# Kernel tuning notes

Hardware: AMD Instinct MI355X
Metric: run time of the kernel (lower is better)

The kernel has to match this reference:

```python
import jax, jax.numpy as jnp
import numpy as np

N_NODES = 50000
N_EDGES = 800000
D = 64


def setup_inputs() -> dict:
    key = jax.random.key(0)
    ks = jax.random.split(key, 8)
    x = jax.random.normal(ks[0], (N_NODES, D), dtype=jnp.float32)
    edge_index = jax.random.randint(ks[1], (2, N_EDGES), 0, N_NODES, dtype=jnp.int64)
    # GCNConv params (PyG: Linear without bias inside lin, bias added after aggregation)
    def glorot(k, fan_in, fan_out):
        lim = (6.0 / (fan_in + fan_out)) ** 0.5
        return jax.random.uniform(k, (fan_in, fan_out), jnp.float32, -lim, lim)
    W1 = glorot(ks[2], D, D); b1 = jnp.zeros((D,), jnp.float32)
    W2 = glorot(ks[3], D, D); b2 = jnp.zeros((D,), jnp.float32)
    W3 = glorot(ks[4], D, D); b3 = jnp.zeros((D,), jnp.float32)
    return {"x": x, "edge_index": edge_index,
            "W1": W1, "b1": b1, "W2": W2, "b2": b2, "W3": W3, "b3": b3}


def _gcn_norm(edge_index, n_nodes, dtype):
    # Add self-loops, compute symmetric normalization D^-1/2 (A+I) D^-1/2 (PyG GCNConv default).
    loop = jnp.arange(n_nodes, dtype=edge_index.dtype)
    src = jnp.concatenate([edge_index[0], loop])  # message source j
    dst = jnp.concatenate([edge_index[1], loop])  # aggregation target i
    deg = jax.ops.segment_sum(jnp.ones_like(dst, dtype=dtype), dst, num_segments=n_nodes)
    dinv = jnp.where(deg > 0, jax.lax.rsqrt(deg), 0.0)
    norm = dinv[src] * dinv[dst]  # [E + N]
    return src, dst, norm


def _gcn_conv(x, src, dst, norm, W, b, n_nodes):
    h = x @ W                              # [N, D_out]
    msg = h[src] * norm[:, None]           # gather + scale, [E+N, D_out]
    out = jax.ops.segment_sum(msg, dst, num_segments=n_nodes)  # scatter-add
    return out + b


def reference(x, edge_index, W1, b1, W2, b2, W3, b3):
    n = x.shape[0]
    src, dst, norm = _gcn_norm(edge_index, n, x.dtype)
    # layer 0: conv -> relu -> residual
    h = _gcn_conv(x, src, dst, norm, W1, b1, n)
    h = jax.nn.relu(h) + x
    # layer 1: conv -> relu -> residual
    r = h
    h = _gcn_conv(h, src, dst, norm, W2, b2, n)
    h = jax.nn.relu(h) + r
    # layer 2 (final): conv only
    h = _gcn_conv(h, src, dst, norm, W3, b3, n)
    return h
```

## Files before the change

kernel.cpp:

```cpp
#include <hip/hip_runtime.h>
#include <hip/hip_bf16.h>


#define CAP 64
#define EDGE_CHUNK 1024

typedef __attribute__((ext_vector_type(8))) short bf16x8;
typedef __attribute__((ext_vector_type(4))) float f32x4;

__device__ inline unsigned pack_bf16(float a, float b) {
    union { float f; unsigned i; } ua, ub;
    ua.f = a; ub.f = b;
    unsigned x = (ua.i + 0x7fffu + ((ua.i >> 16) & 1u)) >> 16;
    unsigned y = (ub.i + 0x7fffu + ((ub.i >> 16) & 1u)) >> 16;
    return x | (y << 16);
}
__device__ inline unsigned short to_bf16(float a) {
    union { float f; unsigned i; } u; u.f = a;
    return (unsigned short)((u.i + 0x7fffu + ((u.i >> 16) & 1u)) >> 16);
}
__device__ inline void acc_bf16x2(unsigned u, float& a, float& b) {
    union { unsigned i; float f; } lo, hi;
    lo.i = u << 16;
    hi.i = u & 0xffff0000u;
    a += lo.f; b += hi.f;
}

__global__ void fill_kernel(const int* __restrict__ src, const int* __restrict__ dst,
                            int* __restrict__ cnt, int* __restrict__ adj,
                            int E, int npc) {
    int cls = blockIdx.x & 7;
    int base = (blockIdx.x >> 3) * EDGE_CHUNK;
    int end = min(base + EDGE_CHUNK, E);
    int lo = cls * npc, hi = lo + npc;
    for (int e = base + threadIdx.x; e < end; e += blockDim.x) {
        int d = dst[e];
        if (d >= lo && d < hi) {
            int p = atomicAdd(&cnt[d], 1);
            adj[(size_t)d * CAP + p] = src[e];
        }
    }
}

__device__ inline void stage_W(const float* __restrict__ W, unsigned short* Wb, int t) {
#pragma unroll
    for (int e0 = 0; e0 < 2; e0++) {
        int e = t + e0 * 256;
        int sc = e >> 6;
        int l  = e & 63;
        int s = sc >> 2, c = sc & 3;
        int nn = c * 16 + (l & 15);
        int kb = s * 32 + (l >> 4) * 8;
        const float* wp = &W[(size_t)kb * 64 + nn];
        unsigned q0 = pack_bf16(wp[0 * 64], wp[1 * 64]);
        unsigned q1 = pack_bf16(wp[2 * 64], wp[3 * 64]);
        unsigned q2 = pack_bf16(wp[4 * 64], wp[5 * 64]);
        unsigned q3 = pack_bf16(wp[6 * 64], wp[7 * 64]);
        *(uint4*)&Wb[e * 8] = make_uint4(q0, q1, q2, q3);
    }
}

__global__ __launch_bounds__(256) void gemm_kernel(const float* __restrict__ in,
                                                   const float* __restrict__ W,
                                                   const int* __restrict__ cnt,
                                                   unsigned short* __restrict__ g, int n) {
    __shared__ unsigned short Wb[512 * 8];
    int t = threadIdx.x;
    stage_W(W, Wb, t);

    int wv = t >> 6;
    int lane = t & 63;
    int quad = lane >> 4;
    int m16 = lane & 15;

    int rowA = blockIdx.x * 64 + wv * 16 + m16;
    union { bf16x8 v; uint4 u; } a0, a1;
    {
        float4 f0 = make_float4(0, 0, 0, 0), f1 = f0, f2 = f0, f3 = f0;
        if (rowA < n) {
            const float* rp = &in[(size_t)rowA * 64];
            f0 = *(const float4*)&rp[quad * 8];
            f1 = *(const float4*)&rp[quad * 8 + 4];
            f2 = *(const float4*)&rp[32 + quad * 8];
            f3 = *(const float4*)&rp[32 + quad * 8 + 4];
        }
        a0.u = make_uint4(pack_bf16(f0.x, f0.y), pack_bf16(f0.z, f0.w),
                          pack_bf16(f1.x, f1.y), pack_bf16(f1.z, f1.w));
        a1.u = make_uint4(pack_bf16(f2.x, f2.y), pack_bf16(f2.z, f2.w),
                          pack_bf16(f3.x, f3.y), pack_bf16(f3.z, f3.w));
    }
    __syncthreads();

    f32x4 acc[4];
#pragma unroll
    for (int c = 0; c < 4; c++) {
        bf16x8 b0 = *(const bf16x8*)&Wb[((size_t)(0 * 4 + c) * 64 + lane) * 8];
        bf16x8 b1 = *(const bf16x8*)&Wb[((size_t)(1 * 4 + c) * 64 + lane) * 8];
        f32x4 z = {0.f, 0.f, 0.f, 0.f};
        z = __builtin_amdgcn_mfma_f32_16x16x32_bf16(a0.v, b0, z, 0, 0, 0);
        z = __builtin_amdgcn_mfma_f32_16x16x32_bf16(a1.v, b1, z, 0, 0, 0);
        acc[c] = z;
    }

    int rowbase = blockIdx.x * 64 + wv * 16 + quad * 4;
    float dv[4];
#pragma unroll
    for (int r = 0; r < 4; r++) {
        int row = rowbase + r;
        dv[r] = (row < n) ? rsqrtf((float)(cnt[row] + 1)) : 0.f;
    }
#pragma unroll
    for (int c = 0; c < 4; c++) {
#pragma unroll
        for (int r = 0; r < 4; r++) {
            int row = rowbase + r;
            if (row < n)
                g[(size_t)row * 64 + c * 16 + m16] = to_bf16(acc[c][r] * dv[r]);
        }
    }
}

template <int WRITE_H>
__global__ __launch_bounds__(256, 4) void aggemm_kernel(
        const unsigned short* __restrict__ g_in,
        const int* __restrict__ cnt,
        const int* __restrict__ adj,
        const float* __restrict__ bias,
        const float* __restrict__ res,
        const float* __restrict__ W,
        float* __restrict__ h_out,
        unsigned short* __restrict__ g_out,
        int n) {
    __shared__ unsigned short Wb[512 * 8];
    __shared__ unsigned short Afrag[256 * 8];
    __shared__ float dsh[32];
    int t = threadIdx.x;

    int r  = t >> 3;
    int lg = t & 7;
    const int c8 = lg * 8;
    int i = blockIdx.x * 32 + r;
    float v0 = 0.f, v1 = 0.f, v2 = 0.f, v3 = 0.f;
    float v4 = 0.f, v5 = 0.f, v6 = 0.f, v7 = 0.f;
    float dvv = 0.f;
    if (i < n) {
        int deg = cnt[i];
        const int* lst = adj + (size_t)i * CAP;
        float4 rr0 = *(const float4*)&res[(size_t)i * 64 + c8];
        float4 rr1 = *(const float4*)&res[(size_t)i * 64 + c8 + 4];
        float a0 = 0.f, a1 = 0.f, a2 = 0.f, a3 = 0.f;
        float a4 = 0.f, a5 = 0.f, a6 = 0.f, a7 = 0.f;
        {
            uint4 v = *(const uint4*)&g_in[(size_t)i * 64 + c8];
            acc_bf16x2(v.x, a0, a1); acc_bf16x2(v.y, a2, a3);
            acc_bf16x2(v.z, a4, a5); acc_bf16x2(v.w, a6, a7);
        }
        int nfull = deg >> 3;
        int4 ja, jb;
        if (nfull > 0) { ja = *(const int4*)&lst[0]; jb = *(const int4*)&lst[4]; }
        for (int b = 0; b < nfull; b++) {
            int4 na = ja, nb = jb;
            if (b + 1 < nfull) {
                na = *(const int4*)&lst[(b + 1) * 8];
                nb = *(const int4*)&lst[(b + 1) * 8 + 4];
            }
            uint4 w0 = *(const uint4*)&g_in[(size_t)ja.x * 64 + c8];
            uint4 w1 = *(const uint4*)&g_in[(size_t)ja.y * 64 + c8];
            uint4 w2 = *(const uint4*)&g_in[(size_t)ja.z * 64 + c8];
            uint4 w3 = *(const uint4*)&g_in[(size_t)ja.w * 64 + c8];
            uint4 w4 = *(const uint4*)&g_in[(size_t)jb.x * 64 + c8];
            uint4 w5 = *(const uint4*)&g_in[(size_t)jb.y * 64 + c8];
            uint4 w6 = *(const uint4*)&g_in[(size_t)jb.z * 64 + c8];
            uint4 w7 = *(const uint4*)&g_in[(size_t)jb.w * 64 + c8];
            acc_bf16x2(w0.x, a0, a1); acc_bf16x2(w0.y, a2, a3);
            acc_bf16x2(w0.z, a4, a5); acc_bf16x2(w0.w, a6, a7);
            acc_bf16x2(w1.x, a0, a1); acc_bf16x2(w1.y, a2, a3);
            acc_bf16x2(w1.z, a4, a5); acc_bf16x2(w1.w, a6, a7);
            acc_bf16x2(w2.x, a0, a1); acc_bf16x2(w2.y, a2, a3);
            acc_bf16x2(w2.z, a4, a5); acc_bf16x2(w2.w, a6, a7);
            acc_bf16x2(w3.x, a0, a1); acc_bf16x2(w3.y, a2, a3);
            acc_bf16x2(w3.z, a4, a5); acc_bf16x2(w3.w, a6, a7);
            acc_bf16x2(w4.x, a0, a1); acc_bf16x2(w4.y, a2, a3);
            acc_bf16x2(w4.z, a4, a5); acc_bf16x2(w4.w, a6, a7);
            acc_bf16x2(w5.x, a0, a1); acc_bf16x2(w5.y, a2, a3);
            acc_bf16x2(w5.z, a4, a5); acc_bf16x2(w5.w, a6, a7);
            acc_bf16x2(w6.x, a0, a1); acc_bf16x2(w6.y, a2, a3);
            acc_bf16x2(w6.z, a4, a5); acc_bf16x2(w6.w, a6, a7);
            acc_bf16x2(w7.x, a0, a1); acc_bf16x2(w7.y, a2, a3);
            acc_bf16x2(w7.z, a4, a5); acc_bf16x2(w7.w, a6, a7);
            ja = na; jb = nb;
        }
        int k = nfull * 8;
        if (k + 4 <= deg) {
            int4 j4 = *(const int4*)&lst[k];
            uint4 w0 = *(const uint4*)&g_in[(size_t)j4.x * 64 + c8];
            uint4 w1 = *(const uint4*)&g_in[(size_t)j4.y * 64 + c8];
            uint4 w2 = *(const uint4*)&g_in[(size_t)j4.z * 64 + c8];
            uint4 w3 = *(const uint4*)&g_in[(size_t)j4.w * 64 + c8];
            acc_bf16x2(w0.x, a0, a1); acc_bf16x2(w0.y, a2, a3);
            acc_bf16x2(w0.z, a4, a5); acc_bf16x2(w0.w, a6, a7);
            acc_bf16x2(w1.x, a0, a1); acc_bf16x2(w1.y, a2, a3);
            acc_bf16x2(w1.z, a4, a5); acc_bf16x2(w1.w, a6, a7);
            acc_bf16x2(w2.x, a0, a1); acc_bf16x2(w2.y, a2, a3);
            acc_bf16x2(w2.z, a4, a5); acc_bf16x2(w2.w, a6, a7);
            acc_bf16x2(w3.x, a0, a1); acc_bf16x2(w3.y, a2, a3);
            acc_bf16x2(w3.z, a4, a5); acc_bf16x2(w3.w, a6, a7);
            k += 4;
        }
        for (; k < deg; k++) {
            uint4 v = *(const uint4*)&g_in[(size_t)lst[k] * 64 + c8];
            acc_bf16x2(v.x, a0, a1); acc_bf16x2(v.y, a2, a3);
            acc_bf16x2(v.z, a4, a5); acc_bf16x2(v.w, a6, a7);
        }
        dvv = rsqrtf((float)(deg + 1));
        float4 b0 = *(const float4*)&bias[c8];
        float4 b1 = *(const float4*)&bias[c8 + 4];
        v0 = fmaxf(dvv * a0 + b0.x, 0.f) + rr0.x;
        v1 = fmaxf(dvv * a1 + b0.y, 0.f) + rr0.y;
        v2 = fmaxf(dvv * a2 + b0.z, 0.f) + rr0.z;
        v3 = fmaxf(dvv * a3 + b0.w, 0.f) + rr0.w;
        v4 = fmaxf(dvv * a4 + b1.x, 0.f) + rr1.x;
        v5 = fmaxf(dvv * a5 + b1.y, 0.f) + rr1.y;
        v6 = fmaxf(dvv * a6 + b1.z, 0.f) + rr1.z;
        v7 = fmaxf(dvv * a7 + b1.w, 0.f) + rr1.w;
        if (WRITE_H) {
            *(float4*)&h_out[(size_t)i * 64 + c8]     = make_float4(v0, v1, v2, v3);
            *(float4*)&h_out[(size_t)i * 64 + c8 + 4] = make_float4(v4, v5, v6, v7);
        }
    }
    stage_W(W, Wb, t);
    {
        uint4 pk;
        pk.x = pack_bf16(v0, v1);
        pk.y = pack_bf16(v2, v3);
        pk.z = pack_bf16(v4, v5);
        pk.w = pack_bf16(v6, v7);
        int sA = r >> 4, mA = r & 15;
        *(uint4*)&Afrag[((size_t)(sA * 8 + lg) * 16 + mA) * 8] = pk;
        if (lg == 0) dsh[r] = dvv;
    }
    __syncthreads();

    int wv = t >> 6;
    int lane = t & 63;
    int quad = lane >> 4;
    int m16 = lane & 15;
    int sB = wv & 1;
    int ch = wv >> 1;
    bf16x8 af0 = *(const bf16x8*)&Afrag[((size_t)(sB * 8 + quad) * 16 + m16) * 8];
    bf16x8 af1 = *(const bf16x8*)&Afrag[((size_t)(sB * 8 + 4 + quad) * 16 + m16) * 8];
    f32x4 acc[2];
#pragma unroll
    for (int c2 = 0; c2 < 2; c2++) {
        int c = ch * 2 + c2;
        bf16x8 b0 = *(const bf16x8*)&Wb[((size_t)(0 * 4 + c) * 64 + lane) * 8];
        bf16x8 b1 = *(const bf16x8*)&Wb[((size_t)(1 * 4 + c) * 64 + lane) * 8];
        f32x4 z = {0.f, 0.f, 0.f, 0.f};
        z = __builtin_amdgcn_mfma_f32_16x16x32_bf16(af0, b0, z, 0, 0, 0);
        z = __builtin_amdgcn_mfma_f32_16x16x32_bf16(af1, b1, z, 0, 0, 0);
        acc[c2] = z;
    }
    int lrow = sB * 16 + quad * 4;
    int rowbase = blockIdx.x * 32 + lrow;
    float dv2[4];
#pragma unroll
    for (int rr = 0; rr < 4; rr++)
        dv2[rr] = dsh[lrow + rr];
#pragma unroll
    for (int c2 = 0; c2 < 2; c2++) {
        int c = ch * 2 + c2;
#pragma unroll
        for (int rr = 0; rr < 4; rr++) {
            int row = rowbase + rr;
            if (row < n)
                g_out[(size_t)row * 64 + c * 16 + m16] = to_bf16(acc[c2][rr] * dv2[rr]);
        }
    }
}

__global__ __launch_bounds__(256, 4) void agg_kernel(const unsigned short* __restrict__ g,
                                                     const int* __restrict__ cnt,
                                                     const int* __restrict__ adj,
                                                     const float* __restrict__ bias,
                                                     float* __restrict__ out, int n) {
    int t = threadIdx.x;
    int lg = t & 7;
    int i = blockIdx.x * 32 + (t >> 3);
    if (i >= n) return;
    int deg = cnt[i];
    const int* lst = adj + (size_t)i * CAP;
    const int c8 = lg * 8;
    size_t rowoff = (size_t)i * 64 + c8;
    float a0 = 0.f, a1 = 0.f, a2 = 0.f, a3 = 0.f;
    float a4 = 0.f, a5 = 0.f, a6 = 0.f, a7 = 0.f;
    {
        uint4 v = *(const uint4*)&g[(size_t)i * 64 + c8];
        acc_bf16x2(v.x, a0, a1); acc_bf16x2(v.y, a2, a3);
        acc_bf16x2(v.z, a4, a5); acc_bf16x2(v.w, a6, a7);
    }
    int nfull = deg >> 3;
    int4 ja, jb;
    if (nfull > 0) { ja = *(const int4*)&lst[0]; jb = *(const int4*)&lst[4]; }
    for (int b = 0; b < nfull; b++) {
        int4 na = ja, nb = jb;
        if (b + 1 < nfull) {
            na = *(const int4*)&lst[(b + 1) * 8];
            nb = *(const int4*)&lst[(b + 1) * 8 + 4];
        }
        uint4 v0 = *(const uint4*)&g[(size_t)ja.x * 64 + c8];
        uint4 v1 = *(const uint4*)&g[(size_t)ja.y * 64 + c8];
        uint4 v2 = *(const uint4*)&g[(size_t)ja.z * 64 + c8];
        uint4 v3 = *(const uint4*)&g[(size_t)ja.w * 64 + c8];
        uint4 v4 = *(const uint4*)&g[(size_t)jb.x * 64 + c8];
        uint4 v5 = *(const uint4*)&g[(size_t)jb.y * 64 + c8];
        uint4 v6 = *(const uint4*)&g[(size_t)jb.z * 64 + c8];
        uint4 v7 = *(const uint4*)&g[(size_t)jb.w * 64 + c8];
        acc_bf16x2(v0.x, a0, a1); acc_bf16x2(v0.y, a2, a3);
        acc_bf16x2(v0.z, a4, a5); acc_bf16x2(v0.w, a6, a7);
        acc_bf16x2(v1.x, a0, a1); acc_bf16x2(v1.y, a2, a3);
        acc_bf16x2(v1.z, a4, a5); acc_bf16x2(v1.w, a6, a7);
        acc_bf16x2(v2.x, a0, a1); acc_bf16x2(v2.y, a2, a3);
        acc_bf16x2(v2.z, a4, a5); acc_bf16x2(v2.w, a6, a7);
        acc_bf16x2(v3.x, a0, a1); acc_bf16x2(v3.y, a2, a3);
        acc_bf16x2(v3.z, a4, a5); acc_bf16x2(v3.w, a6, a7);
        acc_bf16x2(v4.x, a0, a1); acc_bf16x2(v4.y, a2, a3);
        acc_bf16x2(v4.z, a4, a5); acc_bf16x2(v4.w, a6, a7);
        acc_bf16x2(v5.x, a0, a1); acc_bf16x2(v5.y, a2, a3);
        acc_bf16x2(v5.z, a4, a5); acc_bf16x2(v5.w, a6, a7);
        acc_bf16x2(v6.x, a0, a1); acc_bf16x2(v6.y, a2, a3);
        acc_bf16x2(v6.z, a4, a5); acc_bf16x2(v6.w, a6, a7);
        acc_bf16x2(v7.x, a0, a1); acc_bf16x2(v7.y, a2, a3);
        acc_bf16x2(v7.z, a4, a5); acc_bf16x2(v7.w, a6, a7);
        ja = na; jb = nb;
    }
    int k = nfull * 8;
    if (k + 4 <= deg) {
        int4 j4 = *(const int4*)&lst[k];
        uint4 v0 = *(const uint4*)&g[(size_t)j4.x * 64 + c8];
        uint4 v1 = *(const uint4*)&g[(size_t)j4.y * 64 + c8];
        uint4 v2 = *(const uint4*)&g[(size_t)j4.z * 64 + c8];
        uint4 v3 = *(const uint4*)&g[(size_t)j4.w * 64 + c8];
        acc_bf16x2(v0.x, a0, a1); acc_bf16x2(v0.y, a2, a3);
        acc_bf16x2(v0.z, a4, a5); acc_bf16x2(v0.w, a6, a7);
        acc_bf16x2(v1.x, a0, a1); acc_bf16x2(v1.y, a2, a3);
        acc_bf16x2(v1.z, a4, a5); acc_bf16x2(v1.w, a6, a7);
        acc_bf16x2(v2.x, a0, a1); acc_bf16x2(v2.y, a2, a3);
        acc_bf16x2(v2.z, a4, a5); acc_bf16x2(v2.w, a6, a7);
        acc_bf16x2(v3.x, a0, a1); acc_bf16x2(v3.y, a2, a3);
        acc_bf16x2(v3.z, a4, a5); acc_bf16x2(v3.w, a6, a7);
        k += 4;
    }
    for (; k < deg; k++) {
        uint4 v = *(const uint4*)&g[(size_t)lst[k] * 64 + c8];
        acc_bf16x2(v.x, a0, a1); acc_bf16x2(v.y, a2, a3);
        acc_bf16x2(v.z, a4, a5); acc_bf16x2(v.w, a6, a7);
    }
    float dv = rsqrtf((float)(deg + 1));
    float4 b0 = *(const float4*)&bias[c8];
    float4 b1 = *(const float4*)&bias[c8 + 4];
    float4 o0, o1;
    o0.x = dv * a0 + b0.x; o0.y = dv * a1 + b0.y;
    o0.z = dv * a2 + b0.z; o0.w = dv * a3 + b0.w;
    o1.x = dv * a4 + b1.x; o1.y = dv * a5 + b1.y;
    o1.z = dv * a6 + b1.z; o1.w = dv * a7 + b1.w;
    *(float4*)&out[rowoff] = o0;
    *(float4*)&out[rowoff + 4] = o1;
}

extern "C" void kernel_launch(void* const* d_in, const int* in_sizes, int n_in,
                              void* d_out, int out_size, void* d_ws, size_t ws_size,
                              hipStream_t stream) {
    const float* x  = (const float*)d_in[0];
    const int*   ei = (const int*)d_in[1];
    const float* W1 = (const float*)d_in[2];
    const float* b1 = (const float*)d_in[3];
    const float* W2 = (const float*)d_in[4];
    const float* b2 = (const float*)d_in[5];
    const float* W3 = (const float*)d_in[6];
    const float* b3 = (const float*)d_in[7];
    float* out = (float*)d_out;

    const int N = in_sizes[0] / 64;
    const int E = in_sizes[1] / 2;
    const int* src = ei;
    const int* dst = ei + E;
    const int npc = (N + 7) / 8;
    const int nEdgeChunks = (E + EDGE_CHUNK - 1) / EDGE_CHUNK;

    char* p = (char*)d_ws;
    int*            cnt = (int*)p;            p += ((N + 63) / 64) * 64 * 4;
    int*            adj = (int*)p;            p += ((size_t)N + 1) * CAP * 4;
    unsigned short* ga  = (unsigned short*)p; p += (size_t)N * 64 * 2;
    unsigned short* gb  = (unsigned short*)p; p += (size_t)N * 64 * 2;
    float*          h1  = (float*)p;          p += (size_t)N * 64 * 4;

    const int tileBlocks = (N + 63) / 64;
    const int halfBlocks = (N + 31) / 32;

    hipMemsetAsync(cnt, 0, (size_t)N * 4, stream);
    fill_kernel<<<nEdgeChunks * 8, 256, 0, stream>>>(src, dst, cnt, adj, E, npc);

    gemm_kernel<<<tileBlocks, 256, 0, stream>>>(x, W1, cnt, ga, N);
    aggemm_kernel<1><<<halfBlocks, 256, 0, stream>>>(ga, cnt, adj, b1, x, W2, h1, gb, N);
    aggemm_kernel<0><<<halfBlocks, 256, 0, stream>>>(gb, cnt, adj, b2, h1, W3, nullptr, ga, N);
    agg_kernel<<<halfBlocks, 256, 0, stream>>>(ga, cnt, adj, b3, out, N);
}
```

Measured before the change: 182.4 us.

## Software-pipeline neighbor gathers, stage GEMM outputs through LDS, store residual as bf16

The per-row neighbor gather moves into a shared helper that prefetches the next batch of eight neighbor rows and the index batch after that while the current batch accumulates, to hide gather latency. The GEMM and fused agg-GEMM kernels now stage their bf16 output tile in shared memory and write full 16-byte rows, replacing the earlier scattered 2-byte stores. The intermediate residual h1 is kept as bf16 instead of fp32, halving its write and read traffic at some cost in precision. The gemm kernel also gets a launch-bounds occupancy hint, and extra barriers are added to reuse shared buffers.

```diff
diff --git a/kernel.cpp b/kernel.cpp
--- a/kernel.cpp
+++ b/kernel.cpp
@@ -24,6 +24,83 @@
     lo.i = u << 16;
     hi.i = u & 0xffff0000u;
     a += lo.f; b += hi.f;
+}
+
+__device__ inline void gather_rows(const unsigned short* __restrict__ g,
+                                   const int* __restrict__ lst, int deg, int c8,
+                                   float& a0, float& a1, float& a2, float& a3,
+                                   float& a4, float& a5, float& a6, float& a7) {
+    int nfull = deg >> 3;
+    int4 ja, jb, na, nb;
+    uint4 w0, w1, w2, w3, w4, w5, w6, w7;
+    if (nfull > 0) {
+        ja = *(const int4*)&lst[0]; jb = *(const int4*)&lst[4];
+        w0 = *(const uint4*)&g[(size_t)ja.x * 64 + c8];
+        w1 = *(const uint4*)&g[(size_t)ja.y * 64 + c8];
+        w2 = *(const uint4*)&g[(size_t)ja.z * 64 + c8];
+        w3 = *(const uint4*)&g[(size_t)ja.w * 64 + c8];
+        w4 = *(const uint4*)&g[(size_t)jb.x * 64 + c8];
+        w5 = *(const uint4*)&g[(size_t)jb.y * 64 + c8];
+        w6 = *(const uint4*)&g[(size_t)jb.z * 64 + c8];
+        w7 = *(const uint4*)&g[(size_t)jb.w * 64 + c8];
+        if (nfull > 1) { na = *(const int4*)&lst[8]; nb = *(const int4*)&lst[12]; }
+    }
+    for (int b = 0; b < nfull; b++) {
+        bool has1 = (b + 1 < nfull);
+        bool has2 = (b + 2 < nfull);
+        int4 ta, tb;
+        if (has2) {
+            ta = *(const int4*)&lst[(b + 2) * 8];
+            tb = *(const int4*)&lst[(b + 2) * 8 + 4];
+        }
+        acc_bf16x2(w0.x, a0, a1); acc_bf16x2(w0.y, a2, a3);
+        acc_bf16x2(w0.z, a4, a5); acc_bf16x2(w0.w, a6, a7);
+        if (has1) w0 = *(const uint4*)&g[(size_t)na.x * 64 + c8];
+        acc_bf16x2(w1.x, a0, a1); acc_bf16x2(w1.y, a2, a3);
+        acc_bf16x2(w1.z, a4, a5); acc_bf16x2(w1.w, a6, a7);
+        if (has1) w1 = *(const uint4*)&g[(size_t)na.y * 64 + c8];
+        acc_bf16x2(w2.x, a0, a1); acc_bf16x2(w2.y, a2, a3);
+        acc_bf16x2(w2.z, a4, a5); acc_bf16x2(w2.w, a6, a7);
+        if (has1) w2 = *(const uint4*)&g[(size_t)na.z * 64 + c8];
+        acc_bf16x2(w3.x, a0, a1); acc_bf16x2(w3.y, a2, a3);
+        acc_bf16x2(w3.z, a4, a5); acc_bf16x2(w3.w, a6, a7);
+        if (has1) w3 = *(const uint4*)&g[(size_t)na.w * 64 + c8];
+        acc_bf16x2(w4.x, a0, a1); acc_bf16x2(w4.y, a2, a3);
+        acc_bf16x2(w4.z, a4, a5); acc_bf16x2(w4.w, a6, a7);
+        if (has1) w4 = *(const uint4*)&g[(size_t)nb.x * 64 + c8];
+        acc_bf16x2(w5.x, a0, a1); acc_bf16x2(w5.y, a2, a3);
+        acc_bf16x2(w5.z, a4, a5); acc_bf16x2(w5.w, a6, a7);
+        if (has1) w5 = *(const uint4*)&g[(size_t)nb.y * 64 + c8];
+        acc_bf16x2(w6.x, a0, a1); acc_bf16x2(w6.y, a2, a3);
+        acc_bf16x2(w6.z, a4, a5); acc_bf16x2(w6.w, a6, a7);
+        if (has1) w6 = *(const uint4*)&g[(size_t)nb.z * 64 + c8];
+        acc_bf16x2(w7.x, a0, a1); acc_bf16x2(w7.y, a2, a3);
+        acc_bf16x2(w7.z, a4, a5); acc_bf16x2(w7.w, a6, a7);
+        if (has1) w7 = *(const uint4*)&g[(size_t)nb.w * 64 + c8];
+        if (has2) { na = ta; nb = tb; }
+    }
+    int k = nfull * 8;
+    if (k + 4 <= deg) {
+        int4 j4 = *(const int4*)&lst[k];
+        uint4 t0 = *(const uint4*)&g[(size_t)j4.x * 64 + c8];
+        uint4 t1 = *(const uint4*)&g[(size_t)j4.y * 64 + c8];
+        uint4 t2 = *(const uint4*)&g[(size_t)j4.z * 64 + c8];
+        uint4 t3 = *(const uint4*)&g[(size_t)j4.w * 64 + c8];
+        acc_bf16x2(t0.x, a0, a1); acc_bf16x2(t0.y, a2, a3);
+        acc_bf16x2(t0.z, a4, a5); acc_bf16x2(t0.w, a6, a7);
+        acc_bf16x2(t1.x, a0, a1); acc_bf16x2(t1.y, a2, a3);
+        acc_bf16x2(t1.z, a4, a5); acc_bf16x2(t1.w, a6, a7);
+        acc_bf16x2(t2.x, a0, a1); acc_bf16x2(t2.y, a2, a3);
+        acc_bf16x2(t2.z, a4, a5); acc_bf16x2(t2.w, a6, a7);
+        acc_bf16x2(t3.x, a0, a1); acc_bf16x2(t3.y, a2, a3);
+        acc_bf16x2(t3.z, a4, a5); acc_bf16x2(t3.w, a6, a7);
+        k += 4;
+    }
+    for (; k < deg; k++) {
+        uint4 v = *(const uint4*)&g[(size_t)lst[k] * 64 + c8];
+        acc_bf16x2(v.x, a0, a1); acc_bf16x2(v.y, a2, a3);
+        acc_bf16x2(v.z, a4, a5); acc_bf16x2(v.w, a6, a7);
+    }
 }
 
 __global__ void fill_kernel(const int* __restrict__ src, const int* __restrict__ dst,
@@ -60,10 +137,10 @@
     }
 }
 
-__global__ __launch_bounds__(256) void gemm_kernel(const float* __restrict__ in,
-                                                   const float* __restrict__ W,
-                                                   const int* __restrict__ cnt,
-                                                   unsigned short* __restrict__ g, int n) {
+__global__ __launch_bounds__(256, 4) void gemm_kernel(const float* __restrict__ in,
+                                                      const float* __restrict__ W,
+                                                      const int* __restrict__ cnt,
+                                                      unsigned short* __restrict__ g, int n) {
     __shared__ unsigned short Wb[512 * 8];
     int t = threadIdx.x;
     stage_W(W, Wb, t);
@@ -102,37 +179,46 @@
         acc[c] = z;
     }
 
-    int rowbase = blockIdx.x * 64 + wv * 16 + quad * 4;
+    int lrow = wv * 16 + quad * 4;
     float dv[4];
 #pragma unroll
     for (int r = 0; r < 4; r++) {
-        int row = rowbase + r;
+        int row = blockIdx.x * 64 + lrow + r;
         dv[r] = (row < n) ? rsqrtf((float)(cnt[row] + 1)) : 0.f;
     }
+    __syncthreads();
+    unsigned short* Ofrag = Wb;
 #pragma unroll
     for (int c = 0; c < 4; c++) {
 #pragma unroll
-        for (int r = 0; r < 4; r++) {
-            int row = rowbase + r;
-            if (row < n)
-                g[(size_t)row * 64 + c * 16 + m16] = to_bf16(acc[c][r] * dv[r]);
-        }
-    }
-}
-
-template <int WRITE_H>
+        for (int r = 0; r < 4; r++)
+            Ofrag[(size_t)(lrow + r) * 64 + c * 16 + m16] = to_bf16(acc[c][r] * dv[r]);
+    }
+    __syncthreads();
+#pragma unroll
+    for (int it = 0; it < 2; it++) {
+        int unit = t + it * 256;
+        int row = unit >> 3, chv = unit & 7;
+        int grow = blockIdx.x * 64 + row;
+        if (grow < n)
+            *(uint4*)&g[(size_t)grow * 64 + chv * 8] =
+                *(const uint4*)&Ofrag[(size_t)row * 64 + chv * 8];
+    }
+}
+
+template <int WRITE_H, int RES_BF16>
 __global__ __launch_bounds__(256, 4) void aggemm_kernel(
         const unsigned short* __restrict__ g_in,
         const int* __restrict__ cnt,
         const int* __restrict__ adj,
         const float* __restrict__ bias,
-        const float* __restrict__ res,
+        const void* __restrict__ res_p,
         const float* __restrict__ W,
-        float* __restrict__ h_out,
+        unsigned short* __restrict__ h_out,
         unsigned short* __restrict__ g_out,
         int n) {
     __shared__ unsigned short Wb[512 * 8];
-    __shared__ unsigned short Afrag[256 * 8];
+    __shared__ unsigned short Afrag[2048];
     __shared__ float dsh[32];
     int t = threadIdx.x;
 
@@ -146,8 +232,20 @@
     if (i < n) {
         int deg = cnt[i];
         const int* lst = adj + (size_t)i * CAP;
-        float4 rr0 = *(const float4*)&res[(size_t)i * 64 + c8];
-        float4 rr1 = *(const float4*)&res[(size_t)i * 64 + c8 + 4];
+        float r0 = 0.f, r1 = 0.f, r2 = 0.f, r3 = 0.f;
+        float r4 = 0.f, r5 = 0.f, r6 = 0.f, r7 = 0.f;
+        if (RES_BF16) {
+            const unsigned short* rp = (const unsigned short*)res_p;
+            uint4 rv = *(const uint4*)&rp[(size_t)i * 64 + c8];
+            acc_bf16x2(rv.x, r0, r1); acc_bf16x2(rv.y, r2, r3);
+            acc_bf16x2(rv.z, r4, r5); acc_bf16x2(rv.w, r6, r7);
+        } else {
+            const float* rp = (const float*)res_p;
+            float4 q0 = *(const float4*)&rp[(size_t)i * 64 + c8];
+            float4 q1 = *(const float4*)&rp[(size_t)i * 64 + c8 + 4];
+            r0 = q0.x; r1 = q0.y; r2 = q0.z; r3 = q0.w;
+            r4 = q1.x; r5 = q1.y; r6 = q1.z; r7 = q1.w;
+        }
         float a0 = 0.f, a1 = 0.f, a2 = 0.f, a3 = 0.f;
         float a4 = 0.f, a5 = 0.f, a6 = 0.f, a7 = 0.f;
         {
@@ -155,86 +253,28 @@
             acc_bf16x2(v.x, a0, a1); acc_bf16x2(v.y, a2, a3);
             acc_bf16x2(v.z, a4, a5); acc_bf16x2(v.w, a6, a7);
         }
-        int nfull = deg >> 3;
-        int4 ja, jb;
-        if (nfull > 0) { ja = *(const int4*)&lst[0]; jb = *(const int4*)&lst[4]; }
-        for (int b = 0; b < nfull; b++) {
-            int4 na = ja, nb = jb;
-            if (b + 1 < nfull) {
-                na = *(const int4*)&lst[(b + 1) * 8];
-                nb = *(const int4*)&lst[(b + 1) * 8 + 4];
-            }
-            uint4 w0 = *(const uint4*)&g_in[(size_t)ja.x * 64 + c8];
-            uint4 w1 = *(const uint4*)&g_in[(size_t)ja.y * 64 + c8];
-            uint4 w2 = *(const uint4*)&g_in[(size_t)ja.z * 64 + c8];
-            uint4 w3 = *(const uint4*)&g_in[(size_t)ja.w * 64 + c8];
-            uint4 w4 = *(const uint4*)&g_in[(size_t)jb.x * 64 + c8];
-            uint4 w5 = *(const uint4*)&g_in[(size_t)jb.y * 64 + c8];
-            uint4 w6 = *(const uint4*)&g_in[(size_t)jb.z * 64 + c8];
-            uint4 w7 = *(const uint4*)&g_in[(size_t)jb.w * 64 + c8];
-            acc_bf16x2(w0.x, a0, a1); acc_bf16x2(w0.y, a2, a3);
-            acc_bf16x2(w0.z, a4, a5); acc_bf16x2(w0.w, a6, a7);
-            acc_bf16x2(w1.x, a0, a1); acc_bf16x2(w1.y, a2, a3);
-            acc_bf16x2(w1.z, a4, a5); acc_bf16x2(w1.w, a6, a7);
-            acc_bf16x2(w2.x, a0, a1); acc_bf16x2(w2.y, a2, a3);
-            acc_bf16x2(w2.z, a4, a5); acc_bf16x2(w2.w, a6, a7);
-            acc_bf16x2(w3.x, a0, a1); acc_bf16x2(w3.y, a2, a3);
-            acc_bf16x2(w3.z, a4, a5); acc_bf16x2(w3.w, a6, a7);
-            acc_bf16x2(w4.x, a0, a1); acc_bf16x2(w4.y, a2, a3);
-            acc_bf16x2(w4.z, a4, a5); acc_bf16x2(w4.w, a6, a7);
-            acc_bf16x2(w5.x, a0, a1); acc_bf16x2(w5.y, a2, a3);
-            acc_bf16x2(w5.z, a4, a5); acc_bf16x2(w5.w, a6, a7);
-            acc_bf16x2(w6.x, a0, a1); acc_bf16x2(w6.y, a2, a3);
-            acc_bf16x2(w6.z, a4, a5); acc_bf16x2(w6.w, a6, a7);
-            acc_bf16x2(w7.x, a0, a1); acc_bf16x2(w7.y, a2, a3);
-            acc_bf16x2(w7.z, a4, a5); acc_bf16x2(w7.w, a6, a7);
-            ja = na; jb = nb;
-        }
-        int k = nfull * 8;
-        if (k + 4 <= deg) {
-            int4 j4 = *(const int4*)&lst[k];
-            uint4 w0 = *(const uint4*)&g_in[(size_t)j4.x * 64 + c8];
-            uint4 w1 = *(const uint4*)&g_in[(size_t)j4.y * 64 + c8];
-            uint4 w2 = *(const uint4*)&g_in[(size_t)j4.z * 64 + c8];
-            uint4 w3 = *(const uint4*)&g_in[(size_t)j4.w * 64 + c8];
-            acc_bf16x2(w0.x, a0, a1); acc_bf16x2(w0.y, a2, a3);
-            acc_bf16x2(w0.z, a4, a5); acc_bf16x2(w0.w, a6, a7);
-            acc_bf16x2(w1.x, a0, a1); acc_bf16x2(w1.y, a2, a3);
-            acc_bf16x2(w1.z, a4, a5); acc_bf16x2(w1.w, a6, a7);
-            acc_bf16x2(w2.x, a0, a1); acc_bf16x2(w2.y, a2, a3);
-            acc_bf16x2(w2.z, a4, a5); acc_bf16x2(w2.w, a6, a7);
-            acc_bf16x2(w3.x, a0, a1); acc_bf16x2(w3.y, a2, a3);
-            acc_bf16x2(w3.z, a4, a5); acc_bf16x2(w3.w, a6, a7);
-            k += 4;
-        }
-        for (; k < deg; k++) {
-            uint4 v = *(const uint4*)&g_in[(size_t)lst[k] * 64 + c8];
-            acc_bf16x2(v.x, a0, a1); acc_bf16x2(v.y, a2, a3);
-            acc_bf16x2(v.z, a4, a5); acc_bf16x2(v.w, a6, a7);
-        }
+        gather_rows(g_in, lst, deg, c8, a0, a1, a2, a3, a4, a5, a6, a7);
         dvv = rsqrtf((float)(deg + 1));
         float4 b0 = *(const float4*)&bias[c8];
         float4 b1 = *(const float4*)&bias[c8 + 4];
-        v0 = fmaxf(dvv * a0 + b0.x, 0.f) + rr0.x;
-        v1 = fmaxf(dvv * a1 + b0.y, 0.f) + rr0.y;
-        v2 = fmaxf(dvv * a2 + b0.z, 0.f) + rr0.z;
-        v3 = fmaxf(dvv * a3 + b0.w, 0.f) + rr0.w;
-        v4 = fmaxf(dvv * a4 + b1.x, 0.f) + rr1.x;
-        v5 = fmaxf(dvv * a5 + b1.y, 0.f) + rr1.y;
-        v6 = fmaxf(dvv * a6 + b1.z, 0.f) + rr1.z;
-        v7 = fmaxf(dvv * a7 + b1.w, 0.f) + rr1.w;
-        if (WRITE_H) {
-            *(float4*)&h_out[(size_t)i * 64 + c8]     = make_float4(v0, v1, v2, v3);
-            *(float4*)&h_out[(size_t)i * 64 + c8 + 4] = make_float4(v4, v5, v6, v7);
-        }
-    }
+        v0 = fmaxf(dvv * a0 + b0.x, 0.f) + r0;
+        v1 = fmaxf(dvv * a1 + b0.y, 0.f) + r1;
+        v2 = fmaxf(dvv * a2 + b0.z, 0.f) + r2;
+        v3 = fmaxf(dvv * a3 + b0.w, 0.f) + r3;
+        v4 = fmaxf(dvv * a4 + b1.x, 0.f) + r4;
+        v5 = fmaxf(dvv * a5 + b1.y, 0.f) + r5;
+        v6 = fmaxf(dvv * a6 + b1.z, 0.f) + r6;
+        v7 = fmaxf(dvv * a7 + b1.w, 0.f) + r7;
+    }
+    uint4 pk;
+    pk.x = pack_bf16(v0, v1);
+    pk.y = pack_bf16(v2, v3);
+    pk.z = pack_bf16(v4, v5);
+    pk.w = pack_bf16(v6, v7);
+    if (WRITE_H && i < n)
+        *(uint4*)&h_out[(size_t)i * 64 + c8] = pk;
     stage_W(W, Wb, t);
     {
-        uint4 pk;
-        pk.x = pack_bf16(v0, v1);
-        pk.y = pack_bf16(v2, v3);
-        pk.z = pack_bf16(v4, v5);
-        pk.w = pack_bf16(v6, v7);
         int sA = r >> 4, mA = r & 15;
         *(uint4*)&Afrag[((size_t)(sA * 8 + lg) * 16 + mA) * 8] = pk;
         if (lg == 0) dsh[r] = dvv;
@@ -249,6 +289,12 @@
     int ch = wv >> 1;
     bf16x8 af0 = *(const bf16x8*)&Afrag[((size_t)(sB * 8 + quad) * 16 + m16) * 8];
     bf16x8 af1 = *(const bf16x8*)&Afrag[((size_t)(sB * 8 + 4 + quad) * 16 + m16) * 8];
+    int lrow = sB * 16 + quad * 4;
+    float dv2[4];
+#pragma unroll
+    for (int rr = 0; rr < 4; rr++)
+        dv2[rr] = dsh[lrow + rr];
+    __syncthreads();
     f32x4 acc[2];
 #pragma unroll
     for (int c2 = 0; c2 < 2; c2++) {
@@ -260,21 +306,19 @@
         z = __builtin_amdgcn_mfma_f32_16x16x32_bf16(af1, b1, z, 0, 0, 0);
         acc[c2] = z;
     }
-    int lrow = sB * 16 + quad * 4;
-    int rowbase = blockIdx.x * 32 + lrow;
-    float dv2[4];
-#pragma unroll
-    for (int rr = 0; rr < 4; rr++)
-        dv2[rr] = dsh[lrow + rr];
 #pragma unroll
     for (int c2 = 0; c2 < 2; c2++) {
         int c = ch * 2 + c2;
 #pragma unroll
-        for (int rr = 0; rr < 4; rr++) {
-            int row = rowbase + rr;
-            if (row < n)
-                g_out[(size_t)row * 64 + c * 16 + m16] = to_bf16(acc[c2][rr] * dv2[rr]);
-        }
+        for (int rr = 0; rr < 4; rr++)
+            Afrag[(size_t)(lrow + rr) * 64 + c * 16 + m16] = to_bf16(acc[c2][rr] * dv2[rr]);
+    }
+    __syncthreads();
+    {
+        int orow = blockIdx.x * 32 + r;
+        if (orow < n)
+            *(uint4*)&g_out[(size_t)orow * 64 + c8] =
+                *(const uint4*)&Afrag[(size_t)r * 64 + c8];
     }
 }
 
@@ -298,63 +342,7 @@
         acc_bf16x2(v.x, a0, a1); acc_bf16x2(v.y, a2, a3);
         acc_bf16x2(v.z, a4, a5); acc_bf16x2(v.w, a6, a7);
     }
-    int nfull = deg >> 3;
-    int4 ja, jb;
-    if (nfull > 0) { ja = *(const int4*)&lst[0]; jb = *(const int4*)&lst[4]; }
-    for (int b = 0; b < nfull; b++) {
-        int4 na = ja, nb = jb;
-        if (b + 1 < nfull) {
-            na = *(const int4*)&lst[(b + 1) * 8];
-            nb = *(const int4*)&lst[(b + 1) * 8 + 4];
-        }
-        uint4 v0 = *(const uint4*)&g[(size_t)ja.x * 64 + c8];
-        uint4 v1 = *(const uint4*)&g[(size_t)ja.y * 64 + c8];
-        uint4 v2 = *(const uint4*)&g[(size_t)ja.z * 64 + c8];
-        uint4 v3 = *(const uint4*)&g[(size_t)ja.w * 64 + c8];
-        uint4 v4 = *(const uint4*)&g[(size_t)jb.x * 64 + c8];
-        uint4 v5 = *(const uint4*)&g[(size_t)jb.y * 64 + c8];
-        uint4 v6 = *(const uint4*)&g[(size_t)jb.z * 64 + c8];
-        uint4 v7 = *(const uint4*)&g[(size_t)jb.w * 64 + c8];
-        acc_bf16x2(v0.x, a0, a1); acc_bf16x2(v0.y, a2, a3);
-        acc_bf16x2(v0.z, a4, a5); acc_bf16x2(v0.w, a6, a7);
-        acc_bf16x2(v1.x, a0, a1); acc_bf16x2(v1.y, a2, a3);
-        acc_bf16x2(v1.z, a4, a5); acc_bf16x2(v1.w, a6, a7);
-        acc_bf16x2(v2.x, a0, a1); acc_bf16x2(v2.y, a2, a3);
-        acc_bf16x2(v2.z, a4, a5); acc_bf16x2(v2.w, a6, a7);
-        acc_bf16x2(v3.x, a0, a1); acc_bf16x2(v3.y, a2, a3);
-        acc_bf16x2(v3.z, a4, a5); acc_bf16x2(v3.w, a6, a7);
-        acc_bf16x2(v4.x, a0, a1); acc_bf16x2(v4.y, a2, a3);
-        acc_bf16x2(v4.z, a4, a5); acc_bf16x2(v4.w, a6, a7);
-        acc_bf16x2(v5.x, a0, a1); acc_bf16x2(v5.y, a2, a3);
-        acc_bf16x2(v5.z, a4, a5); acc_bf16x2(v5.w, a6, a7);
-        acc_bf16x2(v6.x, a0, a1); acc_bf16x2(v6.y, a2, a3);
-        acc_bf16x2(v6.z, a4, a5); acc_bf16x2(v6.w, a6, a7);
-        acc_bf16x2(v7.x, a0, a1); acc_bf16x2(v7.y, a2, a3);
-        acc_bf16x2(v7.z, a4, a5); acc_bf16x2(v7.w, a6, a7);
-        ja = na; jb = nb;
-    }
-    int k = nfull * 8;
-    if (k + 4 <= deg) {
-        int4 j4 = *(const int4*)&lst[k];
-        uint4 v0 = *(const uint4*)&g[(size_t)j4.x * 64 + c8];
-        uint4 v1 = *(const uint4*)&g[(size_t)j4.y * 64 + c8];
-        uint4 v2 = *(const uint4*)&g[(size_t)j4.z * 64 + c8];
-        uint4 v3 = *(const uint4*)&g[(size_t)j4.w * 64 + c8];
-        acc_bf16x2(v0.x, a0, a1); acc_bf16x2(v0.y, a2, a3);
-        acc_bf16x2(v0.z, a4, a5); acc_bf16x2(v0.w, a6, a7);
-        acc_bf16x2(v1.x, a0, a1); acc_bf16x2(v1.y, a2, a3);
-        acc_bf16x2(v1.z, a4, a5); acc_bf16x2(v1.w, a6, a7);
-        acc_bf16x2(v2.x, a0, a1); acc_bf16x2(v2.y, a2, a3);
-        acc_bf16x2(v2.z, a4, a5); acc_bf16x2(v2.w, a6, a7);
-        acc_bf16x2(v3.x, a0, a1); acc_bf16x2(v3.y, a2, a3);
-        acc_bf16x2(v3.z, a4, a5); acc_bf16x2(v3.w, a6, a7);
-        k += 4;
-    }
-    for (; k < deg; k++) {
-        uint4 v = *(const uint4*)&g[(size_t)lst[k] * 64 + c8];
-        acc_bf16x2(v.x, a0, a1); acc_bf16x2(v.y, a2, a3);
-        acc_bf16x2(v.z, a4, a5); acc_bf16x2(v.w, a6, a7);
-    }
+    gather_rows(g, lst, deg, c8, a0, a1, a2, a3, a4, a5, a6, a7);
     float dv = rsqrtf((float)(deg + 1));
     float4 b0 = *(const float4*)&bias[c8];
     float4 b1 = *(const float4*)&bias[c8 + 4];
@@ -388,11 +376,12 @@
     const int nEdgeChunks = (E + EDGE_CHUNK - 1) / EDGE_CHUNK;
 
     char* p = (char*)d_ws;
-    int*            cnt = (int*)p;            p += ((N + 63) / 64) * 64 * 4;
+    const int Na = ((N + 63) / 64) * 64;
+    int*            cnt = (int*)p;            p += (size_t)Na * 4;
     int*            adj = (int*)p;            p += ((size_t)N + 1) * CAP * 4;
     unsigned short* ga  = (unsigned short*)p; p += (size_t)N * 64 * 2;
     unsigned short* gb  = (unsigned short*)p; p += (size_t)N * 64 * 2;
-    float*          h1  = (float*)p;          p += (size_t)N * 64 * 4;
+    unsigned short* h1  = (unsigned short*)p; p += (size_t)N * 64 * 2;
 
     const int tileBlocks = (N + 63) / 64;
     const int halfBlocks = (N + 31) / 32;
@@ -401,7 +390,9 @@
     fill_kernel<<<nEdgeChunks * 8, 256, 0, stream>>>(src, dst, cnt, adj, E, npc);
 
     gemm_kernel<<<tileBlocks, 256, 0, stream>>>(x, W1, cnt, ga, N);
-    aggemm_kernel<1><<<halfBlocks, 256, 0, stream>>>(ga, cnt, adj, b1, x, W2, h1, gb, N);
-    aggemm_kernel<0><<<halfBlocks, 256, 0, stream>>>(gb, cnt, adj, b2, h1, W3, nullptr, ga, N);
+    aggemm_kernel<1, 0><<<halfBlocks, 256, 0, stream>>>(ga, cnt, adj, b1, (const void*)x,
+                                                        W2, h1, gb, N);
+    aggemm_kernel<0, 1><<<halfBlocks, 256, 0, stream>>>(gb, cnt, adj, b2, (const void*)h1,
+                                                        W3, nullptr, ga, N);
     agg_kernel<<<halfBlocks, 256, 0, stream>>>(ga, cnt, adj, b3, out, N);
 }
```

Result: no change. 182.4 us (+0.0%).
